# Kernel optimization log

Hardware: AMD Instinct MI355X
Metric: run time of the kernel (lower is better)

The kernel has to match this reference:

```python
import jax, jax.numpy as jnp
import numpy as np
import math
from jax import lax

D_MODEL = 128
N_HEADS = 8
D_HEAD = D_MODEL // N_HEADS
D_FF = 4 * D_MODEL
KERNEL = 25  # moving_avg kernel size
N_LAYERS = 2
EPS = 1e-5


def moving_avg(x):
    # x: [B, L, D]; replicate-pad (KERNEL-1)//2 at both ends, window mean (AvgPool1d stride 1)
    p = (KERNEL - 1) // 2
    xp = jnp.concatenate([jnp.repeat(x[:, :1], p, axis=1), x, jnp.repeat(x[:, -1:], p, axis=1)], axis=1)
    s = lax.reduce_window(xp, 0.0, lax.add, (1, KERNEL, 1), (1, 1, 1), 'VALID')
    return s / KERNEL


def series_decomp(x):
    mm = moving_avg(x)
    return x - mm, mm


def autocorrelation(q, k, v):
    # q,k,v: [B, L, H, E]; FFT-based period correlation + top-k time-delay aggregation (training path)
    B, L, H, E = q.shape
    top_k = int(1 * math.log(L))  # factor=1
    qf = jnp.fft.rfft(q.transpose(0, 2, 3, 1), axis=-1)
    kf = jnp.fft.rfft(k.transpose(0, 2, 3, 1), axis=-1)
    corr = jnp.fft.irfft(qf * jnp.conj(kf), n=L, axis=-1)  # [B, H, E, L]
    vals = v.transpose(0, 2, 3, 1)                          # [B, H, E, L]
    mean_value = corr.mean(axis=(1, 2))                     # [B, L]
    _, index = lax.top_k(mean_value.mean(axis=0), top_k)    # [top_k], lags shared over batch
    weights = mean_value[:, index]                          # [B, top_k]
    tmp_corr = jax.nn.softmax(weights, axis=-1)
    agg = jnp.zeros_like(vals)
    for i in range(top_k):  # static small loop (top_k = 8)
        pattern = jnp.roll(vals, -index[i], axis=-1)
        agg = agg + pattern * tmp_corr[:, i][:, None, None, None]
    return agg.transpose(0, 3, 1, 2)  # [B, L, H, E]


def attn_layer(x, w, b):
    # w: [4, D, D] (q,k,v,out torch-Linear weights), b: [4, D]
    B, L, D = x.shape
    q = (jnp.einsum('bld,ed->ble', x, w[0]) + b[0]).reshape(B, L, N_HEADS, D_HEAD)
    k = (jnp.einsum('bld,ed->ble', x, w[1]) + b[1]).reshape(B, L, N_HEADS, D_HEAD)
    v = (jnp.einsum('bld,ed->ble', x, w[2]) + b[2]).reshape(B, L, N_HEADS, D_HEAD)
    o = autocorrelation(q, k, v).reshape(B, L, D)
    return jnp.einsum('bld,ed->ble', o, w[3]) + b[3]


def encoder_layer(x, w, b, w1, w2):
    x = x + attn_layer(x, w, b)
    x, _ = series_decomp(x)
    y = jax.nn.gelu(jnp.einsum('bld,fd->blf', x, w1), approximate=False)  # conv1 (k=1, no bias)
    y = jnp.einsum('blf,df->bld', y, w2)                                   # conv2 (k=1, no bias)
    res, _ = series_decomp(x + y)
    return res


def reference(x_enc, emb_w, attn_w, attn_b, ffn_w1, ffn_w2, norm_g, norm_b, fc1_w, fc1_b, fc2_w, fc2_b):
    # token embedding: Conv1d(C -> D, kernel 3, circular padding, no bias)
    xc = x_enc.transpose(0, 2, 1)  # [B, C, L]
    xc = jnp.concatenate([xc[:, :, -1:], xc, xc[:, :, :1]], axis=-1)
    h = lax.conv_general_dilated(xc, emb_w, (1,), 'VALID', dimension_numbers=('NCH', 'OIH', 'NCH'))
    h = h.transpose(0, 2, 1)  # [B, L, D]
    for l in range(N_LAYERS):
        h = encoder_layer(h, attn_w[l], attn_b[l], ffn_w1[l], ffn_w2[l])
    # my_Layernorm: LayerNorm then subtract time-mean
    mu = h.mean(axis=-1, keepdims=True)
    var = ((h - mu) ** 2).mean(axis=-1, keepdims=True)
    ln = (h - mu) / jnp.sqrt(var + EPS) * norm_g + norm_b
    h = ln - ln.mean(axis=1, keepdims=True)
    # head: gelu -> mean pool over time -> MLP
    h = jax.nn.gelu(h, approximate=False).mean(axis=1)  # [B, D]
    h = jax.nn.relu(jnp.einsum('bd,hd->bh', h, fc1_w) + fc1_b)
    return jnp.einsum('bh,ch->bc', h, fc2_w) + fc2_b


def setup_inputs() -> dict:
    key = jax.random.key(0)
    ks = jax.random.split(key, 8)
    B, L, C, NC, FC = 32, 4096, 12, 5, 128
    s = 0.02
    return {
        'x_enc': jax.random.normal(ks[0], (B, L, C), jnp.float32),
        'emb_w': jax.random.normal(ks[1], (D_MODEL, C, 3), jnp.float32) * s,
        'attn_w': jax.random.normal(ks[2], (N_LAYERS, 4, D_MODEL, D_MODEL), jnp.float32) * s,
        'attn_b': jnp.zeros((N_LAYERS, 4, D_MODEL), jnp.float32),
        'ffn_w1': jax.random.normal(ks[3], (N_LAYERS, D_FF, D_MODEL), jnp.float32) * s,
        'ffn_w2': jax.random.normal(ks[4], (N_LAYERS, D_MODEL, D_FF), jnp.float32) * s,
        'norm_g': jnp.ones((D_MODEL,), jnp.float32),
        'norm_b': jnp.zeros((D_MODEL,), jnp.float32),
        'fc1_w': jax.random.normal(ks[5], (FC, D_MODEL), jnp.float32) * s,
        'fc1_b': jnp.zeros((FC,), jnp.float32),
        'fc2_w': jax.random.normal(ks[6], (NC, FC), jnp.float32) * s,
        'fc2_b': jnp.zeros((NC,), jnp.float32),
    }
```

## Files before the change

### kernel.cpp

```cpp
#include <hip/hip_runtime.h>
#include <math.h>

#define L_SEQ 4096
#define BATCH 32
#define DM 128

typedef short short8 __attribute__((ext_vector_type(8)));
typedef float f32x4 __attribute__((ext_vector_type(4)));

__device__ __forceinline__ float gelu_f(float x) {
    return 0.5f * x * (1.0f + erff(x * 0.70710678118654752f));
}
__device__ __forceinline__ float gelu_fast(float x) {
    float ax = fabsf(x);
    if (ax < 1.0f) {
        float z = x * 0.70710678118654752f;
        float z2 = z * z;
        float p = 1.0f + z2 * (-0.333333333f + z2 * (0.1f + z2 * (-0.0238095238f +
                  z2 * (4.62962963e-3f + z2 * (-7.57575758e-4f)))));
        return 0.5f * x * (1.0f + 1.1283791670955126f * z * p);
    }
    return 0.5f * x * (1.0f + erff(x * 0.70710678118654752f));
}
__device__ __forceinline__ unsigned short f2b(float f) {
    unsigned u = __float_as_uint(f);
    u += 0x7fffu + ((u >> 16) & 1u);
    return (unsigned short)(u >> 16);
}
__device__ __forceinline__ float b2f(unsigned short h) {
    return __uint_as_float(((unsigned)h) << 16);
}

__global__ __launch_bounds__(256) void kembed(const float* __restrict__ x,
                                              const float* __restrict__ w,
                                              float* __restrict__ h) {
    __shared__ float xs[130][12];
    __shared__ float wsm[128][37];
    int b = blockIdx.x >> 5;
    int lt = blockIdx.x & 31;
    int l0 = lt * 128;
    int tid = threadIdx.x;
    for (int i = tid; i < 130 * 12; i += 256) {
        int r = i / 12, c = i - r * 12;
        int gl = (l0 - 1 + r + 4096) & 4095;
        xs[r][c] = x[((size_t)b * 4096 + gl) * 12 + c];
    }
    for (int i = tid; i < 128 * 36; i += 256) {
        int o = i / 36, j = i - o * 36;
        wsm[o][j] = w[i];
    }
    __syncthreads();
    int o = tid & 127, lh = tid >> 7;
    float wr[36];
#pragma unroll
    for (int j = 0; j < 36; j++) wr[j] = wsm[o][j];
    int base_r = lh * 64;
    float ring[4][12];
#pragma unroll
    for (int c = 0; c < 12; c++) { ring[0][c] = xs[base_r][c]; ring[1][c] = xs[base_r + 1][c]; }
    float* hp = h + ((size_t)b * 4096 + l0 + lh * 64) * 128 + o;
#pragma unroll 4
    for (int st = 0; st < 64; st++) {
        int s0 = st & 3, s1 = (st + 1) & 3, s2 = (st + 2) & 3;
#pragma unroll
        for (int c = 0; c < 12; c++) ring[s2][c] = xs[base_r + st + 2][c];
        float s = 0.f;
#pragma unroll
        for (int c = 0; c < 12; c++)
            s += wr[c * 3 + 0] * ring[s0][c] + wr[c * 3 + 1] * ring[s1][c] + wr[c * 3 + 2] * ring[s2][c];
        hp[(size_t)st * 128] = s;
    }
}

__global__ __launch_bounds__(256) void kprepw(const float* __restrict__ w1,
                                              const float* __restrict__ w2,
                                              const float* __restrict__ attn_w,
                                              unsigned short* __restrict__ w1img,
                                              unsigned short* __restrict__ w2img,
                                              unsigned short* __restrict__ qkh,
                                              unsigned short* __restrict__ qkl,
                                              unsigned short* __restrict__ voimg) {
    int t = blockIdx.x * 256 + threadIdx.x;
    if (t < 262144) {
        int layer = t >> 17; int rem = t & 131071;
        if (rem < 65536) {
            int R = rem >> 7, x = rem & 127;
            int g = x >> 3, j = x & 7;
            int srcc = ((g ^ (R & 7)) << 3) + j;
            w1img[(size_t)layer * 65536 + rem] = f2b(w1[(size_t)layer * 65536 + R * 128 + srcc]);
        } else {
            int r2 = rem - 65536;
            int c = r2 >> 13; int D = (r2 >> 6) & 127; int x = r2 & 63;
            int g = x >> 3, j = x & 7;
            int srcf = c * 64 + ((g ^ (D & 7)) << 3) + j;
            w2img[(size_t)layer * 65536 + r2] = f2b(w2[(size_t)layer * 65536 + D * 512 + srcf]);
        }
    } else if (t < 327680) {
        int t2 = t - 262144;
        int layer = t2 >> 15; int rem = t2 & 32767;
        int y = rem >> 14; int rem2 = rem & 16383;
        int r64 = rem2 >> 7; int x = rem2 & 127;
        int r = r64 & 63;
        int g = x >> 3, j = x & 7;
        int srcc = ((g ^ (r & 7)) << 3) + j;
        float v = attn_w[(size_t)layer * 65536 + y * 16384 + r64 * 128 + srcc];
        unsigned short hh = f2b(v);
        qkh[t2] = hh;
        qkl[t2] = f2b(v - b2f(hh));
    } else {
        int t3 = t - 327680;
        int layer = t3 >> 15; int rem = t3 & 32767;
        int mat = rem >> 14; int rem2 = rem & 16383;
        int r = rem2 >> 7; int x = rem2 & 127;
        int g = x >> 3, j = x & 7;
        int srcc = ((g ^ (r & 7)) << 3) + j;
        voimg[t3] = f2b(attn_w[(size_t)layer * 65536 + (2 + mat) * 16384 + r * 128 + srcc]);
    }
}

__global__ __launch_bounds__(256, 2) void kgemm_qk3(const float* __restrict__ A,
                                                    const unsigned short* __restrict__ qkh,
                                                    const unsigned short* __restrict__ qkl,
                                                    const float* __restrict__ ab,
                                                    int half, float* __restrict__ CT) {
    __shared__ __align__(16) char smem[65536];
    short* Ah = (short*)smem;
    short* Al = (short*)(smem + 16384);
    short* Wh = (short*)(smem + 32768);
    short* Wl = (short*)(smem + 49152);
    int y = blockIdx.y;
    const unsigned short* wh = qkh + y * 16384 + half * 8192;
    const unsigned short* wl = qkl + y * 16384 + half * 8192;
    const float* bias = ab + y * 128 + half * 64;
    int row0 = blockIdx.x * 64;
    int tid = threadIdx.x;
#pragma unroll
    for (int u = 0; u < 4; u++) {
        int task = tid + u * 256;
        int r = task >> 4, cg = task & 15;
        int dst = r * 128 + ((cg ^ (r & 7)) << 3);
        const float* src = A + ((size_t)(row0 + r)) * 128 + cg * 8;
        float4 xa = *(const float4*)src, ya = *(const float4*)(src + 4);
        float av[8] = {xa.x, xa.y, xa.z, xa.w, ya.x, ya.y, ya.z, ya.w};
        short8 hi, lo;
#pragma unroll
        for (int j = 0; j < 8; j++) {
            unsigned short h = f2b(av[j]);
            hi[j] = (short)h; lo[j] = (short)f2b(av[j] - b2f(h));
        }
        *(short8*)(Ah + dst) = hi; *(short8*)(Al + dst) = lo;
        int lin = r * 128 + cg * 8;
        *(short8*)(Wh + lin) = *(const short8*)(wh + lin);
        *(short8*)(Wl + lin) = *(const short8*)(wl + lin);
    }
    __syncthreads();
    int l = tid & 63; int w = tid >> 6; int wm = w >> 1, wn = w & 1;
    f32x4 acc[2][2];
#pragma unroll
    for (int i = 0; i < 2; i++)
#pragma unroll
        for (int j = 0; j < 2; j++) acc[i][j] = (f32x4){0.f, 0.f, 0.f, 0.f};
#pragma unroll
    for (int ks = 0; ks < 4; ks++) {
        int cg = ks * 4 + (l >> 4);
        short8 ah[2], al2[2], bh[2], bl[2];
#pragma unroll
        for (int mi = 0; mi < 2; mi++) {
            int rm = wm * 32 + mi * 16 + (l & 15);
            int off = rm * 128 + ((cg ^ (rm & 7)) << 3);
            ah[mi] = *(short8*)(Ah + off); al2[mi] = *(short8*)(Al + off);
        }
#pragma unroll
        for (int ni = 0; ni < 2; ni++) {
            int rn = wn * 32 + ni * 16 + (l & 15);
            int off = rn * 128 + ((cg ^ (rn & 7)) << 3);
            bh[ni] = *(short8*)(Wh + off); bl[ni] = *(short8*)(Wl + off);
        }
#pragma unroll
        for (int mi = 0; mi < 2; mi++)
#pragma unroll
            for (int ni = 0; ni < 2; ni++) {
                acc[mi][ni] = __builtin_amdgcn_mfma_f32_16x16x32_bf16(ah[mi], bh[ni], acc[mi][ni], 0, 0, 0);
                acc[mi][ni] = __builtin_amdgcn_mfma_f32_16x16x32_bf16(ah[mi], bl[ni], acc[mi][ni], 0, 0, 0);
                acc[mi][ni] = __builtin_amdgcn_mfma_f32_16x16x32_bf16(al2[mi], bh[ni], acc[mi][ni], 0, 0, 0);
            }
    }
    __syncthreads();
    float* Dsh = (float*)smem;
#pragma unroll
    for (int mi = 0; mi < 2; mi++)
#pragma unroll
        for (int ni = 0; ni < 2; ni++)
#pragma unroll
            for (int rr = 0; rr < 4; rr++) {
                int m = wm * 32 + mi * 16 + (l >> 4) * 4 + rr;
                int n = wn * 32 + ni * 16 + (l & 15);
                Dsh[n * 68 + m] = acc[mi][ni][rr] + bias[n];
            }
    __syncthreads();
    int b = row0 >> 12; int l0 = row0 & 4095;
    int cbase = y * 64;
#pragma unroll
    for (int u = 0; u < 4; u++) {
        int task = tid + u * 256;
        int c = task >> 4, m4 = (task & 15) * 4;
        float4 v = *(float4*)&Dsh[c * 68 + m4];
        *(float4*)&CT[((size_t)(b * 128 + cbase + c)) * 4096 + l0 + m4] = v;
    }
}

template <int AT, int EPI>
__global__ __launch_bounds__(256, 2) void kgemm_mfma(const void* __restrict__ Ap,
                                                     const unsigned short* __restrict__ Wimg,
                                                     const float* __restrict__ bias,
                                                     const float* __restrict__ res,
                                                     const float* __restrict__ tcb,
                                                     const int* __restrict__ idxb,
                                                     void* __restrict__ outp) {
    __shared__ __align__(16) char smem[65536];
    short* As = (short*)smem;
    short* Ws = (short*)(smem + 32768);
    int tid = threadIdx.x;
    size_t row0 = (size_t)blockIdx.x * 128;
#pragma unroll
    for (int u = 0; u < 8; u++) {
        int g = tid + u * 256;
        int r = g >> 4, cg = g & 15;
        int dsti = r * 128 + ((cg ^ (r & 7)) << 3);
        short8 v;
        if (AT == 0) {
            const float* src = (const float*)Ap + (row0 + r) * 128 + cg * 8;
            float4 x = *(const float4*)src, y = *(const float4*)(src + 4);
            v[0] = f2b(x.x); v[1] = f2b(x.y); v[2] = f2b(x.z); v[3] = f2b(x.w);
            v[4] = f2b(y.x); v[5] = f2b(y.y); v[6] = f2b(y.z); v[7] = f2b(y.w);
        } else {
            const unsigned short* Vb = (const unsigned short*)Ap;
            int b = (int)(row0 >> 12);
            int l0 = (int)(row0 & 4095);
            float accv[8];
#pragma unroll
            for (int j = 0; j < 8; j++) accv[j] = 0.f;
#pragma unroll
            for (int i = 0; i < 8; i++) {
                float wgt = tcb[b * 8 + i];
                int lr = (l0 + r + idxb[i]) & 4095;
                short8 vv = *(const short8*)(Vb + ((size_t)(b * 4096 + lr)) * 128 + cg * 8);
#pragma unroll
                for (int j = 0; j < 8; j++) accv[j] += wgt * b2f((unsigned short)vv[j]);
            }
#pragma unroll
            for (int j = 0; j < 8; j++) v[j] = (short)f2b(accv[j]);
        }
        *(short8*)(As + dsti) = v;
        int lin = r * 128 + cg * 8;
        *(short8*)(Ws + lin) = *(const short8*)(Wimg + lin);
    }
    __syncthreads();
    int l = tid & 63; int w = tid >> 6; int wm = w >> 1, wn = w & 1;
    f32x4 acc[4][4];
#pragma unroll
    for (int i = 0; i < 4; i++)
#pragma unroll
        for (int j = 0; j < 4; j++) acc[i][j] = (f32x4){0.f, 0.f, 0.f, 0.f};
#pragma unroll
    for (int ks = 0; ks < 4; ks++) {
        int cg = ks * 4 + (l >> 4);
        short8 af[4], bf[4];
#pragma unroll
        for (int mi = 0; mi < 4; mi++) {
            int rm = wm * 64 + mi * 16 + (l & 15);
            af[mi] = *(short8*)(As + rm * 128 + ((cg ^ (rm & 7)) << 3));
        }
#pragma unroll
        for (int ni = 0; ni < 4; ni++) {
            int rn = wn * 64 + ni * 16 + (l & 15);
            bf[ni] = *(short8*)(Ws + rn * 128 + ((cg ^ (rn & 7)) << 3));
        }
#pragma unroll
        for (int mi = 0; mi < 4; mi++)
#pragma unroll
            for (int ni = 0; ni < 4; ni++)
                acc[mi][ni] = __builtin_amdgcn_mfma_f32_16x16x32_bf16(af[mi], bf[ni], acc[mi][ni], 0, 0, 0);
    }
    __syncthreads();
    float* Dsh = (float*)smem;
#pragma unroll
    for (int mi = 0; mi < 4; mi++)
#pragma unroll
        for (int ni = 0; ni < 4; ni++)
#pragma unroll
            for (int rr = 0; rr < 4; rr++)
                Dsh[(wm * 64 + mi * 16 + (l >> 4) * 4 + rr) * 128 + wn * 64 + ni * 16 + (l & 15)] = acc[mi][ni][rr];
    __syncthreads();
#pragma unroll
    for (int u = 0; u < 8; u++) {
        int g = tid + u * 256;
        int r = g >> 4, c8 = (g & 15) * 8;
        float vv[8];
#pragma unroll
        for (int j = 0; j < 8; j++) vv[j] = Dsh[r * 128 + c8 + j] + bias[c8 + j];
        if (EPI == 1) {
            const float* rp = res + (row0 + r) * 128 + c8;
#pragma unroll
            for (int j = 0; j < 8; j++) vv[j] += rp[j];
            float* op = (float*)outp + (row0 + r) * 128 + c8;
            *(float4*)op = make_float4(vv[0], vv[1], vv[2], vv[3]);
            *(float4*)(op + 4) = make_float4(vv[4], vv[5], vv[6], vv[7]);
        } else {
            short8 ov;
#pragma unroll
            for (int j = 0; j < 8; j++) ov[j] = (short)f2b(vv[j]);
            *(short8*)((short*)outp + (row0 + r) * 128 + c8) = ov;
        }
    }
}

__global__ __launch_bounds__(256, 2) void kffn_mfma(const float* __restrict__ xs,
                                                    const unsigned short* __restrict__ w1img,
                                                    const unsigned short* __restrict__ w2img,
                                                    float* __restrict__ outp) {
    __shared__ __align__(16) char smem[81920];
    short* xsl = (short*)smem;
    short* w1t = (short*)(smem + 32768);
    short* tt  = (short*)(smem + 49152);
    short* w2t = (short*)(smem + 65536);
    int tid = threadIdx.x;
    size_t row0 = (size_t)blockIdx.x * 128;
#pragma unroll
    for (int u = 0; u < 8; u++) {
        int g = tid + u * 256;
        int r = g >> 4, cg = g & 15;
        const float* src = xs + (row0 + r) * 128 + cg * 8;
        float4 x = *(const float4*)src, y = *(const float4*)(src + 4);
        short8 v;
        v[0] = f2b(x.x); v[1] = f2b(x.y); v[2] = f2b(x.z); v[3] = f2b(x.w);
        v[4] = f2b(y.x); v[5] = f2b(y.y); v[6] = f2b(y.z); v[7] = f2b(y.w);
        *(short8*)(xsl + r * 128 + ((cg ^ (r & 7)) << 3)) = v;
    }
    int l = tid & 63; int w = tid >> 6; int wm = w >> 1, wn = w & 1;
    f32x4 acc2[4][4];
#pragma unroll
    for (int i = 0; i < 4; i++)
#pragma unroll
        for (int j = 0; j < 4; j++) acc2[i][j] = (f32x4){0.f, 0.f, 0.f, 0.f};
    for (int fb = 0; fb < 8; fb++) {
        __syncthreads();
#pragma unroll
        for (int u = 0; u < 4; u++) {
            int task = tid + u * 256;
            int r = task >> 4, cg = task & 15;
            *(short8*)(w1t + r * 128 + cg * 8) =
                *(const short8*)(w1img + ((size_t)(fb * 64 + r)) * 128 + cg * 8);
            int r2 = task >> 3, cg2 = task & 7;
            *(short8*)(w2t + r2 * 64 + cg2 * 8) =
                *(const short8*)(w2img + ((size_t)(fb * 128 + r2)) * 64 + cg2 * 8);
        }
        __syncthreads();
        f32x4 a1[4][2];
#pragma unroll
        for (int i = 0; i < 4; i++)
#pragma unroll
            for (int j = 0; j < 2; j++) a1[i][j] = (f32x4){0.f, 0.f, 0.f, 0.f};
#pragma unroll
        for (int ks = 0; ks < 4; ks++) {
            int cg = ks * 4 + (l >> 4);
            short8 af[4], bf[2];
#pragma unroll
            for (int mi = 0; mi < 4; mi++) {
                int rm = wm * 64 + mi * 16 + (l & 15);
                af[mi] = *(short8*)(xsl + rm * 128 + ((cg ^ (rm & 7)) << 3));
            }
#pragma unroll
            for (int ni = 0; ni < 2; ni++) {
                int rn = wn * 32 + ni * 16 + (l & 15);
                bf[ni] = *(short8*)(w1t + rn * 128 + ((cg ^ (rn & 7)) << 3));
            }
#pragma unroll
            for (int mi = 0; mi < 4; mi++)
#pragma unroll
                for (int ni = 0; ni < 2; ni++)
                    a1[mi][ni] = __builtin_amdgcn_mfma_f32_16x16x32_bf16(af[mi], bf[ni], a1[mi][ni], 0, 0, 0);
        }
#pragma unroll
        for (int mi = 0; mi < 4; mi++)
#pragma unroll
            for (int ni = 0; ni < 2; ni++)
#pragma unroll
                for (int rr = 0; rr < 4; rr++) {
                    int m = wm * 64 + mi * 16 + (l >> 4) * 4 + rr;
                    int f = wn * 32 + ni * 16 + (l & 15);
                    tt[m * 64 + (((f >> 3) ^ (m & 7)) << 3) + (f & 7)] = (short)f2b(gelu_fast(a1[mi][ni][rr]));
                }
        __syncthreads();
#pragma unroll
        for (int ks = 0; ks < 2; ks++) {
            int cg = ks * 4 + (l >> 4);
            short8 af[4], bf[4];
#pragma unroll
            for (int mi = 0; mi < 4; mi++) {
                int rm = wm * 64 + mi * 16 + (l & 15);
                af[mi] = *(short8*)(tt + rm * 64 + ((cg ^ (rm & 7)) << 3));
            }
#pragma unroll
            for (int ni = 0; ni < 4; ni++) {
                int rn = wn * 64 + ni * 16 + (l & 15);
                bf[ni] = *(short8*)(w2t + rn * 64 + ((cg ^ (rn & 7)) << 3));
            }
#pragma unroll
            for (int mi = 0; mi < 4; mi++)
#pragma unroll
                for (int ni = 0; ni < 4; ni++)
                    acc2[mi][ni] = __builtin_amdgcn_mfma_f32_16x16x32_bf16(af[mi], bf[ni], acc2[mi][ni], 0, 0, 0);
        }
    }
    __syncthreads();
    float* Dsh = (float*)smem;
#pragma unroll
    for (int mi = 0; mi < 4; mi++)
#pragma unroll
        for (int ni = 0; ni < 4; ni++)
#pragma unroll
            for (int rr = 0; rr < 4; rr++)
                Dsh[(wm * 64 + mi * 16 + (l >> 4) * 4 + rr) * 128 + wn * 64 + ni * 16 + (l & 15)] = acc2[mi][ni][rr];
    __syncthreads();
#pragma unroll
    for (int u = 0; u < 8; u++) {
        int g = tid + u * 256;
        int r = g >> 4, c8 = (g & 15) * 8;
        const float* rp = xs + (row0 + r) * 128 + c8;
        float* op = outp + (row0 + r) * 128 + c8;
        float4 o0, o1;
        o0.x = Dsh[r * 128 + c8 + 0] + rp[0]; o0.y = Dsh[r * 128 + c8 + 1] + rp[1];
        o0.z = Dsh[r * 128 + c8 + 2] + rp[2]; o0.w = Dsh[r * 128 + c8 + 3] + rp[3];
        o1.x = Dsh[r * 128 + c8 + 4] + rp[4]; o1.y = Dsh[r * 128 + c8 + 5] + rp[5];
        o1.z = Dsh[r * 128 + c8 + 6] + rp[6]; o1.w = Dsh[r * 128 + c8 + 7] + rp[7];
        *(float4*)op = o0; *(float4*)(op + 4) = o1;
    }
}

#define FIDX(a) ((a) + ((a) >> 4))

__device__ __forceinline__ float2 twget(const float2* __restrict__ tw, int a, float sgn) {
    float2 T = tw[a & 1023];
    int hi = (a >> 10) & 3;
    float cs = (hi & 1) ? ((hi & 2) ? T.y : -T.y) : ((hi & 2) ? -T.x : T.x);
    float sn = (hi & 1) ? ((hi & 2) ? -T.x : T.x) : ((hi & 2) ? -T.y : T.y);
    return make_float2(cs, sn * sgn);
}

__device__ void fft4096_r4(float2* __restrict__ b0, float2* __restrict__ b1,
                           const float2* __restrict__ tw, float sgn, int tid) {
    float2* cur = b0; float2* nxt = b1;
#pragma unroll
    for (int t = 0; t < 6; t++) {
        int s = 1 << (t << 1);
        int q = tid & (s - 1);
        int ps = tid - q;
        float2 a0 = cur[FIDX(tid)];
        float2 a1 = cur[FIDX(tid + 1024)];
        float2 a2 = cur[FIDX(tid + 2048)];
        float2 a3 = cur[FIDX(tid + 3072)];
        float t0x = a0.x + a2.x, t0y = a0.y + a2.y;
        float t1x = a0.x - a2.x, t1y = a0.y - a2.y;
        float t2x = a1.x + a3.x, t2y = a1.y + a3.y;
        float t3x = a1.x - a3.x, t3y = a1.y - a3.y;
        float it3x = -sgn * t3y, it3y = sgn * t3x;
        float2 A0 = make_float2(t0x + t2x, t0y + t2y);
        float2 A1 = make_float2(t1x + it3x, t1y + it3y);
        float2 A2 = make_float2(t0x - t2x, t0y - t2y);
        float2 A3 = make_float2(t1x - it3x, t1y - it3y);
        int ob = q + (ps << 2);
        nxt[FIDX(ob)] = A0;
        float2 w1 = twget(tw, ps, sgn);
        float2 w2 = twget(tw, ps * 2, sgn);
        float2 w3 = twget(tw, ps * 3, sgn);
        nxt[FIDX(ob + s)] = make_float2(A1.x * w1.x - A1.y * w1.y, A1.x * w1.y + A1.y * w1.x);
        nxt[FIDX(ob + 2 * s)] = make_float2(A2.x * w2.x - A2.y * w2.y, A2.x * w2.y + A2.y * w2.x);
        nxt[FIDX(ob + 3 * s)] = make_float2(A3.x * w3.x - A3.y * w3.y, A3.x * w3.y + A3.y * w3.x);
        __syncthreads();
        float2* tp = cur; cur = nxt; nxt = tp;
    }
}

__global__ __launch_bounds__(1024) void kfft_fwd(const float* __restrict__ qkT,
                                                 float* __restrict__ Pws, int ghalf) {
    __shared__ float2 bufA[4352];
    __shared__ float2 bufB[4352];
    __shared__ float2 tw[1024];
    int tid = threadIdx.x;
    {
        float sn, cs;
        sincosf(1.5339807878856412e-3f * (float)tid, &sn, &cs);
        tw[tid] = make_float2(cs, sn);
    }
    int b = blockIdx.x >> 3;
    int gl = blockIdx.x & 7;
    float2 pacc[4];
#pragma unroll
    for (int j = 0; j < 4; j++) pacc[j] = make_float2(0.f, 0.f);
    for (int c8 = 0; c8 < 8; c8++) {
        int c = gl * 8 + c8;
        const float* qrow = qkT + ((size_t)(b * 128 + c)) * 4096;
        const float* krow = qkT + ((size_t)(b * 128 + 64 + c)) * 4096;
        __syncthreads();
#pragma unroll
        for (int j = 0; j < 4; j++) {
            int i = tid + j * 1024;
            bufA[FIDX(i)] = make_float2(qrow[i], krow[i]);
        }
        __syncthreads();
        fft4096_r4(bufA, bufB, tw, -1.f, tid);
#pragma unroll
        for (int j = 0; j < 4; j++) {
            int f = tid + j * 1024;
            float2 Zf = bufA[FIDX(f)];
            float2 Zm = bufA[FIDX((4096 - f) & 4095)];
            float Qre = 0.5f * (Zf.x + Zm.x), Qim = 0.5f * (Zf.y - Zm.y);
            float Kre = 0.5f * (Zf.y + Zm.y), Kim = -0.5f * (Zf.x - Zm.x);
            pacc[j].x += Qre * Kre + Qim * Kim;
            pacc[j].y += Qim * Kre - Qre * Kim;
        }
    }
    float2* P = (float2*)Pws + (size_t)(b * 16 + ghalf * 8 + gl) * 4096;
#pragma unroll
    for (int j = 0; j < 4; j++) { int f = tid + j * 1024; P[f] = pacc[j]; }
}

__global__ __launch_bounds__(1024) void kfft_inv(const float* __restrict__ Pws,
                                                 float* __restrict__ meanv) {
    __shared__ float2 bufA[4352];
    __shared__ float2 bufB[4352];
    __shared__ float2 tw[1024];
    int tid = threadIdx.x;
    {
        float sn, cs;
        sincosf(1.5339807878856412e-3f * (float)tid, &sn, &cs);
        tw[tid] = make_float2(cs, sn);
    }
    int b = blockIdx.x;
    const float2* P = (const float2*)Pws + (size_t)b * 16 * 4096;
#pragma unroll
    for (int j = 0; j < 4; j++) {
        int i = tid + j * 1024;
        float2 s = make_float2(0.f, 0.f);
#pragma unroll
        for (int gg = 0; gg < 16; gg++) { float2 v = P[gg * 4096 + i]; s.x += v.x; s.y += v.y; }
        bufA[FIDX(i)] = s;
    }
    __syncthreads();
    fft4096_r4(bufA, bufB, tw, 1.f, tid);
    const float scale = 1.0f / (4096.0f * 128.0f);
#pragma unroll
    for (int j = 0; j < 4; j++) {
        int i = tid + j * 1024;
        meanv[b * 4096 + i] = bufA[FIDX(i)].x * scale;
    }
}

__global__ __launch_bounds__(256) void ktopk(const float* __restrict__ meanv,
                                             int* __restrict__ idxout,
                                             float* __restrict__ tc) {
    __shared__ float cm[4096];
    __shared__ float rv[256];
    __shared__ int ri[256];
    __shared__ int sidx[8];
    for (int c = threadIdx.x; c < 4096; c += 256) {
        float s = 0.f;
        for (int b = 0; b < 32; b++) s += meanv[b * 4096 + c];
        cm[c] = s;
    }
    __syncthreads();
    for (int it = 0; it < 8; it++) {
        float bv = -1e30f; int bi = 0;
        for (int c = threadIdx.x; c < 4096; c += 256) {
            float v = cm[c];
            if (v > bv) { bv = v; bi = c; }
        }
        rv[threadIdx.x] = bv; ri[threadIdx.x] = bi;
        __syncthreads();
        for (int off = 128; off > 0; off >>= 1) {
            if (threadIdx.x < off) {
                float v2 = rv[threadIdx.x + off]; int i2 = ri[threadIdx.x + off];
                if (v2 > rv[threadIdx.x] || (v2 == rv[threadIdx.x] && i2 < ri[threadIdx.x])) {
                    rv[threadIdx.x] = v2; ri[threadIdx.x] = i2;
                }
            }
            __syncthreads();
        }
        if (threadIdx.x == 0) { sidx[it] = ri[0]; idxout[it] = ri[0]; cm[ri[0]] = -1e30f; }
        __syncthreads();
    }
    if (threadIdx.x < 32) {
        int b = threadIdx.x;
        float w[8]; float mx = -1e30f;
#pragma unroll
        for (int i = 0; i < 8; i++) { w[i] = meanv[b * 4096 + sidx[i]]; mx = fmaxf(mx, w[i]); }
        float s = 0.f;
#pragma unroll
        for (int i = 0; i < 8; i++) { w[i] = expf(w[i] - mx); s += w[i]; }
#pragma unroll
        for (int i = 0; i < 8; i++) tc[b * 8 + i] = w[i] / s;
    }
}

__global__ __launch_bounds__(256) void kdecomp(const float* __restrict__ in,
                                               float* __restrict__ outp) {
    int b = blockIdx.x >> 4; int lc = blockIdx.x & 15;
    int dg = threadIdx.x & 31; int ls = threadIdx.x >> 5;
    int l0 = lc * 256 + ls * 32;
    const float* base = in + (size_t)b * 524288 + dg * 4;
    float* ob = outp + (size_t)b * 524288 + dg * 4;
    float sx = 0.f, sy = 0.f, sz = 0.f, sw = 0.f;
#pragma unroll
    for (int j = -12; j <= 12; j++) {
        int lj = l0 + j;
        lj = lj < 0 ? 0 : (lj > 4095 ? 4095 : lj);
        float4 v = *(const float4*)(base + (size_t)lj * 128);
        sx += v.x; sy += v.y; sz += v.z; sw += v.w;
    }
    for (int st = 0; st < 32; st++) {
        int l = l0 + st;
        float4 c = *(const float4*)(base + (size_t)l * 128);
        float4 o = make_float4(c.x - sx * (1.0f / 25.0f), c.y - sy * (1.0f / 25.0f),
                               c.z - sz * (1.0f / 25.0f), c.w - sw * (1.0f / 25.0f));
        *(float4*)(ob + (size_t)l * 128) = o;
        int ln = l + 13 > 4095 ? 4095 : l + 13;
        int lo2 = l - 12 < 0 ? 0 : l - 12;
        float4 vn = *(const float4*)(base + (size_t)ln * 128);
        float4 vo = *(const float4*)(base + (size_t)lo2 * 128);
        sx += vn.x - vo.x; sy += vn.y - vo.y; sz += vn.z - vo.z; sw += vn.w - vo.w;
    }
}

__global__ __launch_bounds__(256) void kln_part1(float* __restrict__ h,
                                                 const float* __restrict__ g,
                                                 const float* __restrict__ bb,
                                                 float* __restrict__ part) {
    __shared__ float sh[4][128];
    int b = blockIdx.x >> 5;
    int sl = blockIdx.x & 31;
    int w = threadIdx.x >> 6;
    int lane = threadIdx.x & 63;
    float2 gv = *(const float2*)(g + lane * 2);
    float2 bv = *(const float2*)(bb + lane * 2);
    size_t r0 = (size_t)b * 4096 + sl * 128 + w * 32;
    float c0 = 0.f, c1 = 0.f;
    for (int i = 0; i < 32; i++) {
        float* p = h + (r0 + i) * 128 + lane * 2;
        float2 v = *(float2*)p;
        float s = v.x + v.y, s2 = v.x * v.x + v.y * v.y;
#pragma unroll
        for (int off = 32; off; off >>= 1) { s += __shfl_down(s, off); s2 += __shfl_down(s2, off); }
        s = __shfl(s, 0); s2 = __shfl(s2, 0);
        float mu = s * (1.f / 128.f);
        float var = s2 * (1.f / 128.f) - mu * mu;
        float inv = rsqrtf(var + 1e-5f);
        float o0 = (v.x - mu) * inv * gv.x + bv.x;
        float o1 = (v.y - mu) * inv * gv.y + bv.y;
        *(float2*)p = make_float2(o0, o1);
        c0 += o0; c1 += o1;
    }
    sh[w][lane * 2] = c0; sh[w][lane * 2 + 1] = c1;
    __syncthreads();
    if (threadIdx.x < 128) {
        int d = threadIdx.x;
        part[(size_t)(b * 32 + sl) * 128 + d] = sh[0][d] + sh[1][d] + sh[2][d] + sh[3][d];
    }
}

__global__ __launch_bounds__(128) void kpart2(const float* __restrict__ part,
                                              float* __restrict__ outm, int nq) {
    int b = blockIdx.x; int d = threadIdx.x;
    float s = 0.f;
    for (int q = 0; q < nq; q++) s += part[(size_t)(b * nq + q) * 128 + d];
    outm[b * 128 + d] = s * (1.f / 4096.f);
}

__global__ __launch_bounds__(256) void kgpart1(const float* __restrict__ h,
                                               const float* __restrict__ msum,
                                               float* __restrict__ part) {
    int b = blockIdx.x >> 3, sl = blockIdx.x & 7;
    int d = threadIdx.x & 127, p = threadIdx.x >> 7;
    const float* base = h + ((size_t)b * 4096 + sl * 512) * 128;
    float m = msum[b * 128 + d];
    float acc = 0.f;
    for (int l = p; l < 512; l += 2) acc += gelu_f(base[(size_t)l * 128 + d] - m);
    __shared__ float sh[256];
    sh[threadIdx.x] = acc; __syncthreads();
    if (p == 0) part[(size_t)(b * 8 + sl) * 128 + d] = acc + sh[128 + d];
}

__global__ __launch_bounds__(256) void khead(const float* __restrict__ gmean,
                                             const float* __restrict__ fc1w,
                                             const float* __restrict__ fc1b,
                                             const float* __restrict__ fc2w,
                                             const float* __restrict__ fc2b,
                                             float* __restrict__ outp) {
    __shared__ float h0[32][128];
    __shared__ float h1[32][128];
    int tid = threadIdx.x;
#pragma unroll
    for (int i = 0; i < 16; i++) {
        int e = tid + i * 256;
        h0[e >> 7][e & 127] = gmean[e];
    }
    __syncthreads();
#pragma unroll
    for (int i = 0; i < 16; i++) {
        int e = tid + i * 256; int b = e >> 7, j = e & 127;
        float s = fc1b[j];
        for (int d = 0; d < 128; d++) s += h0[b][d] * fc1w[j * 128 + d];
        h1[b][j] = fmaxf(s, 0.f);
    }
    __syncthreads();
    if (tid < 160) {
        int b = tid / 5, c2 = tid % 5;
        float s = fc2b[c2];
        for (int j = 0; j < 128; j++) s += h1[b][j] * fc2w[c2 * 128 + j];
        outp[b * 5 + c2] = s;
    }
}

extern "C" void kernel_launch(void* const* d_in, const int* in_sizes, int n_in,
                              void* d_out, int out_size, void* d_ws, size_t ws_size,
                              hipStream_t stream) {
    const float* x_enc  = (const float*)d_in[0];
    const float* emb_w  = (const float*)d_in[1];
    const float* attn_w = (const float*)d_in[2];
    const float* attn_b = (const float*)d_in[3];
    const float* ffn_w1 = (const float*)d_in[4];
    const float* ffn_w2 = (const float*)d_in[5];
    const float* norm_g = (const float*)d_in[6];
    const float* norm_b = (const float*)d_in[7];
    const float* fc1_w  = (const float*)d_in[8];
    const float* fc1_b  = (const float*)d_in[9];
    const float* fc2_w  = (const float*)d_in[10];
    const float* fc2_b  = (const float*)d_in[11];
    float* outp = (float*)d_out;

    float* W = (float*)d_ws;
    const size_t RD = (size_t)BATCH * L_SEQ * DM;
    float* buf0  = W;
    float* buf1  = W + RD;
    float* Pws   = W + 2 * RD;
    float* meanv = Pws + (size_t)4194304;
    float* tcb   = meanv + (size_t)131072;
    int*   idxb  = (int*)(tcb + 256);
    float* part  = tcb + 256 + 64;
    float* msum  = part + 32768;
    float* gsum  = msum + 4096;
    unsigned short* w1img = (unsigned short*)(gsum + 4096);
    unsigned short* w2img = w1img + (size_t)2 * 65536;
    unsigned short* qkh   = w2img + (size_t)2 * 65536;
    unsigned short* qkl   = qkh + (size_t)65536;
    unsigned short* voimg = qkl + (size_t)65536;

    kembed<<<1024, 256, 0, stream>>>(x_enc, emb_w, buf0);
    kprepw<<<1536, 256, 0, stream>>>(ffn_w1, ffn_w2, attn_w, w1img, w2img, qkh, qkl, voimg);

    float* H = buf0;
    float* S = buf1;
    for (int l = 0; l < 2; l++) {
        const float* ab = attn_b + (size_t)l * 4 * 128;
        for (int half = 0; half < 2; half++) {
            kgemm_qk3<<<dim3(2048, 2), 256, 0, stream>>>(H, qkh + (size_t)l * 32768,
                                                         qkl + (size_t)l * 32768, ab, half, S);
            kfft_fwd<<<256, 1024, 0, stream>>>(S, Pws, half);
        }
        kfft_inv<<<32, 1024, 0, stream>>>(Pws, meanv);
        ktopk<<<1, 256, 0, stream>>>(meanv, idxb, tcb);
        unsigned short* Vb = (unsigned short*)S;
        kgemm_mfma<0, 0><<<1024, 256, 0, stream>>>(H, voimg + (size_t)l * 32768, ab + 256,
                                                   nullptr, nullptr, nullptr, Vb);
        kgemm_mfma<2, 1><<<1024, 256, 0, stream>>>(Vb, voimg + (size_t)l * 32768 + 16384, ab + 384,
                                                   H, tcb, idxb, H);
        kdecomp<<<512, 256, 0, stream>>>(H, S);
        kffn_mfma<<<1024, 256, 0, stream>>>(S, w1img + (size_t)l * 65536,
                                            w2img + (size_t)l * 65536, H);
        kdecomp<<<512, 256, 0, stream>>>(H, S);
        float* t = H; H = S; S = t;
    }

    kln_part1<<<1024, 256, 0, stream>>>(H, norm_g, norm_b, meanv);
    kpart2<<<32, 128, 0, stream>>>(meanv, msum, 32);
    kgpart1<<<256, 256, 0, stream>>>(H, msum, part);
    kpart2<<<32, 128, 0, stream>>>(part, gsum, 8);
    khead<<<1, 256, 0, stream>>>(gsum, fc1_w, fc1_b, fc2_w, fc2_b, outp);
}
```

Before: 1.044 ms.

## Double FFT grid parallelism, vectorize loads, split top-k column sum

The forward FFT kernel now launches 512 blocks, each handling 4 channels instead of 8, and the second half accumulates into the first half's partial spectra by read-modify-write rather than writing separate slots. The input staging uses float4 loads instead of scalar strided loads. The batch column sum for top-k moves out of the single-block top-k kernel into a separate 16-block kernel. Together these aim to raise occupancy across the GPU's compute units and shorten the serial single-block phase, at the cost of an extra launch and extra partial-sum traffic.

```diff
diff --git a/kernel.cpp b/kernel.cpp
--- a/kernel.cpp
+++ b/kernel.cpp
@@ -493,21 +493,23 @@
         sincosf(1.5339807878856412e-3f * (float)tid, &sn, &cs);
         tw[tid] = make_float2(cs, sn);
     }
-    int b = blockIdx.x >> 3;
-    int gl = blockIdx.x & 7;
+    int b = blockIdx.x >> 4;
+    int g = blockIdx.x & 15;
     float2 pacc[4];
 #pragma unroll
     for (int j = 0; j < 4; j++) pacc[j] = make_float2(0.f, 0.f);
-    for (int c8 = 0; c8 < 8; c8++) {
-        int c = gl * 8 + c8;
+    for (int c4 = 0; c4 < 4; c4++) {
+        int c = g * 4 + c4;
         const float* qrow = qkT + ((size_t)(b * 128 + c)) * 4096;
         const float* krow = qkT + ((size_t)(b * 128 + 64 + c)) * 4096;
         __syncthreads();
-#pragma unroll
-        for (int j = 0; j < 4; j++) {
-            int i = tid + j * 1024;
-            bufA[FIDX(i)] = make_float2(qrow[i], krow[i]);
-        }
+        int i0 = tid * 4;
+        float4 qv = *(const float4*)(qrow + i0);
+        float4 kv = *(const float4*)(krow + i0);
+        bufA[FIDX(i0)]     = make_float2(qv.x, kv.x);
+        bufA[FIDX(i0 + 1)] = make_float2(qv.y, kv.y);
+        bufA[FIDX(i0 + 2)] = make_float2(qv.z, kv.z);
+        bufA[FIDX(i0 + 3)] = make_float2(qv.w, kv.w);
         __syncthreads();
         fft4096_r4(bufA, bufB, tw, -1.f, tid);
 #pragma unroll
@@ -521,9 +523,18 @@
             pacc[j].y += Qim * Kre - Qre * Kim;
         }
     }
-    float2* P = (float2*)Pws + (size_t)(b * 16 + ghalf * 8 + gl) * 4096;
-#pragma unroll
-    for (int j = 0; j < 4; j++) { int f = tid + j * 1024; P[f] = pacc[j]; }
+    float2* P = (float2*)Pws + (size_t)(b * 16 + g) * 4096;
+    if (ghalf == 0) {
+#pragma unroll
+        for (int j = 0; j < 4; j++) { int f = tid + j * 1024; P[f] = pacc[j]; }
+    } else {
+#pragma unroll
+        for (int j = 0; j < 4; j++) {
+            int f = tid + j * 1024;
+            float2 r = P[f];
+            P[f] = make_float2(r.x + pacc[j].x, r.y + pacc[j].y);
+        }
+    }
 }
 
 __global__ __launch_bounds__(1024) void kfft_inv(const float* __restrict__ Pws,
@@ -557,18 +568,23 @@
     }
 }
 
-__global__ __launch_bounds__(256) void ktopk(const float* __restrict__ meanv,
-                                             int* __restrict__ idxout,
-                                             float* __restrict__ tc) {
+__global__ __launch_bounds__(256) void kcolsum(const float* __restrict__ meanv,
+                                               float* __restrict__ cmg) {
+    int c = blockIdx.x * 256 + threadIdx.x;
+    float s = 0.f;
+    for (int b = 0; b < 32; b++) s += meanv[b * 4096 + c];
+    cmg[c] = s;
+}
+
+__global__ __launch_bounds__(256) void ktopk2(const float* __restrict__ cmg,
+                                              const float* __restrict__ meanv,
+                                              int* __restrict__ idxout,
+                                              float* __restrict__ tc) {
     __shared__ float cm[4096];
     __shared__ float rv[256];
     __shared__ int ri[256];
     __shared__ int sidx[8];
-    for (int c = threadIdx.x; c < 4096; c += 256) {
-        float s = 0.f;
-        for (int b = 0; b < 32; b++) s += meanv[b * 4096 + c];
-        cm[c] = s;
-    }
+    for (int c = threadIdx.x; c < 4096; c += 256) cm[c] = cmg[c];
     __syncthreads();
     for (int it = 0; it < 8; it++) {
         float bv = -1e30f; int bi = 0;
@@ -754,6 +770,7 @@
     unsigned short* qkh   = w2img + (size_t)2 * 65536;
     unsigned short* qkl   = qkh + (size_t)65536;
     unsigned short* voimg = qkl + (size_t)65536;
+    float* cmg   = (float*)(voimg + (size_t)65536);
 
     kembed<<<1024, 256, 0, stream>>>(x_enc, emb_w, buf0);
     kprepw<<<1536, 256, 0, stream>>>(ffn_w1, ffn_w2, attn_w, w1img, w2img, qkh, qkl, voimg);
@@ -765,10 +782,11 @@
         for (int half = 0; half < 2; half++) {
             kgemm_qk3<<<dim3(2048, 2), 256, 0, stream>>>(H, qkh + (size_t)l * 32768,
                                                          qkl + (size_t)l * 32768, ab, half, S);
-            kfft_fwd<<<256, 1024, 0, stream>>>(S, Pws, half);
+            kfft_fwd<<<512, 1024, 0, stream>>>(S, Pws, half);
         }
         kfft_inv<<<32, 1024, 0, stream>>>(Pws, meanv);
-        ktopk<<<1, 256, 0, stream>>>(meanv, idxb, tcb);
+        kcolsum<<<16, 256, 0, stream>>>(meanv, cmg);
+        ktopk2<<<1, 256, 0, stream>>>(cmg, meanv, idxb, tcb);
         unsigned short* Vb = (unsigned short*)S;
         kgemm_mfma<0, 0><<<1024, 256, 0, stream>>>(H, voimg + (size_t)l * 32768, ab + 256,
                                                    nullptr, nullptr, nullptr, Vb);
```

Result: no change. 1.058 ms (+1.4%).
